# Kernel optimization log

Hardware: AMD Instinct MI355X
Metric: run time of the kernel (lower is better)

The kernel has to match this reference:

```python
import jax, jax.numpy as jnp
import numpy as np

D_MODEL = 96
D_INNER = 192   # ssm_ratio * d_model
R = 6           # dt_rank = ceil(96/16)
DH = 32         # d_inner // dt_rank (per-head dim)
K = 4           # scan directions
N = 16          # d_state
EPS = 1e-5


def setup_inputs() -> dict:
    key = jax.random.key(0)
    ks = jax.random.split(key, 10)
    B, H, W = 8, 64, 64
    f = lambda k, s, sc: jax.random.normal(k, s, jnp.float32) * sc
    return dict(
        x=jax.random.normal(ks[0], (B, H, W, D_MODEL), jnp.float32),
        w_in=f(ks[1], (D_MODEL, D_INNER), 0.02),
        w_conv=f(ks[2], (3, 3, 1, D_INNER), 0.1),      # depthwise HWIO
        b_conv=f(ks[3], (D_INNER,), 0.1),
        x_proj_weight=f(ks[4], (K, R + 2 * N, D_INNER), 0.02),
        A_logs=f(ks[5], (K, R), 0.5),
        Ds=jnp.ones((K, R, DH), jnp.float32),
        dt_bias=0.1 * jax.random.uniform(ks[6], (K, R), jnp.float32),
        ln_g=jnp.ones((D_INNER,), jnp.float32),
        ln_b=jnp.zeros((D_INNER,), jnp.float32),
        w_out=f(ks[7], (D_INNER, D_MODEL), 0.02),
    )


def _cross_scan(x):
    # x: (B,H,W,C) -> (B,L,4,C): [row-major, col-major, rev row, rev col]
    B, H, W, C = x.shape
    x0 = x.reshape(B, H * W, C)
    x1 = jnp.transpose(x, (0, 2, 1, 3)).reshape(B, H * W, C)
    return jnp.stack([x0, x1, x0[:, ::-1], x1[:, ::-1]], axis=2)


def _cross_merge(ys, H, W):
    # ys: (B,L,4,C) -> (B,L,C) summed after undoing each scan order
    B, L, _, C = ys.shape
    y_row = ys[:, :, 0] + ys[:, :, 2][:, ::-1]
    y_col = ys[:, :, 1] + ys[:, :, 3][:, ::-1]
    y_col = jnp.transpose(y_col.reshape(B, W, H, C), (0, 2, 1, 3)).reshape(B, L, C)
    return y_row + y_col


def _selective_scan(us, dts, As, Bs, Cs, Dsr, dtb):
    # us:(B,L,KR,DH) dts:(B,L,KR) As:(KR,) Bs,Cs:(B,L,K,N) Dsr:(KR,DH) dtb:(KR,)
    dt = jax.nn.softplus(dts + dtb)                 # (B,L,KR)
    decay = jnp.exp(dt * As)                        # (B,L,KR)
    xu = dt[..., None] * us                         # (B,L,KR,DH)
    Bh = jnp.repeat(Bs, R, axis=2)                  # (B,L,KR,N) head h -> group h//R
    Ch = jnp.repeat(Cs, R, axis=2)
    B_, L, KR, _ = us.shape
    tfirst = lambda a: jnp.moveaxis(a, 1, 0)

    def step(h, inp):
        dec, xu_t, b_t, c_t = inp                   # (B,KR),(B,KR,DH),(B,KR,N),(B,KR,N)
        h = dec[:, :, None, None] * h + xu_t[..., None] * b_t[:, :, None, :]
        y = jnp.einsum('bkdn,bkn->bkd', h, c_t)
        return h, y

    h0 = jnp.zeros((B_, KR, DH, N), us.dtype)
    _, ys = jax.lax.scan(step, h0, (tfirst(decay), tfirst(xu), tfirst(Bh), tfirst(Ch)))
    ys = jnp.moveaxis(ys, 0, 1)                     # (B,L,KR,DH)
    return ys + us * Dsr                            # skip term D*u


def reference(x, w_in, w_conv, b_conv, x_proj_weight, A_logs, Ds, dt_bias, ln_g, ln_b, w_out):
    B, H, W, _ = x.shape
    L = H * W
    xi = x @ w_in                                   # in_proj (no bias)
    xi = jax.lax.conv_general_dilated(
        xi, w_conv, (1, 1), 'SAME', feature_group_count=D_INNER,
        dimension_numbers=('NHWC', 'HWIO', 'NHWC')) + b_conv
    xi = jax.nn.silu(xi)
    xs = _cross_scan(xi)                            # (B,L,4,D_INNER)
    x_dbl = jnp.einsum('blkd,kcd->blkc', xs, x_proj_weight)
    dts = x_dbl[..., :R].reshape(B, L, K * R)
    Bs = x_dbl[..., R:R + N]                        # (B,L,K,N)
    Cs = x_dbl[..., R + N:]
    us = xs.reshape(B, L, K * R, DH)
    As = -jnp.exp(A_logs.astype(jnp.float32)).reshape(K * R)
    Dsr = Ds.reshape(K * R, DH)
    dtb = dt_bias.reshape(K * R)
    ys = _selective_scan(us, dts, As, Bs, Cs, Dsr, dtb)   # (B,L,KR,DH)
    y = _cross_merge(ys.reshape(B, L, K, R * DH), H, W)   # (B,L,D_INNER)
    mu = y.mean(-1, keepdims=True)
    var = ((y - mu) ** 2).mean(-1, keepdims=True)
    y = (y - mu) / jnp.sqrt(var + EPS) * ln_g + ln_b
    y = y.reshape(B, H, W, D_INNER)
    return y @ w_out                                # out_proj (no bias)
```

## Files before the change

### kernel.cpp

```cpp
#include <hip/hip_runtime.h>
#include <hip/hip_bf16.h>

#define BB 8
#define LL 4096
#define DM 96
#define DI 192
#define RRR 6
#define DHH 32
#define KKK 4
#define NNN 16
#define KRR 24
#define NCH 64
#define TT 64
#define RST 48

__device__ __forceinline__ float softplus_f(float x){
    float ax = fabsf(x);
    return fmaxf(x, 0.f) + __logf(1.f + __expf(-ax));
}
__device__ __forceinline__ float silu_f(float x){ return x / (1.f + __expf(-x)); }

__global__ void k0p(const float* __restrict__ W, const float* __restrict__ g,
                    const float* __restrict__ bta, const float* __restrict__ w_out,
                    float* __restrict__ WpR, float* __restrict__ wg, float* __restrict__ sgbw){
    int i = blockIdx.x * 256 + threadIdx.x;
    if (i < DI * 160){
        int d = i / 160, cc = i % 160; int gq = cc / 40, nc = cc % 40;
        int dir = (gq == 0) ? 0 : (gq == 1) ? 2 : (gq == 2) ? 1 : 3;
        float v = 0.f;
        if (nc < 6) v = W[(dir * 38 + nc) * DI + d];
        else if (nc >= 8) v = W[(dir * 38 + (nc - 2)) * DI + d];
        WpR[i] = v;
    } else if (i < DI * 160 + DI * DM){
        int j = i - DI * 160; int c = j / DM;
        wg[j] = w_out[j] * g[c];
    } else if (i < DI * 160 + DI * DM + DM){
        int m = i - (DI * 160 + DI * DM);
        float s = 0.f, t = 0.f;
        for (int c = 0; c < DI; ++c){
            float w = w_out[c * DM + m];
            s = fmaf(g[c], w, s);
            t = fmaf(bta[c], w, t);
        }
        sgbw[m] = s; sgbw[DM + m] = t;
    }
}

__global__ __launch_bounds__(384) void k1_inproj(const float* __restrict__ x,
                                                 const float* __restrict__ w_in,
                                                 float* __restrict__ xw){
    __shared__ float xT[DM][36];
    int pix0 = blockIdx.x * 32;
    for (int i = threadIdx.x; i < 32 * 24; i += 384){
        int c4 = i % 24, p = i / 24;
        float4 v = *(const float4*)(x + (size_t)(pix0 + p) * DM + c4 * 4);
        xT[c4 * 4 + 0][p] = v.x; xT[c4 * 4 + 1][p] = v.y;
        xT[c4 * 4 + 2][p] = v.z; xT[c4 * 4 + 3][p] = v.w;
    }
    __syncthreads();
    int cg = threadIdx.x % 48, pg = threadIdx.x / 48;
    int p0 = pg * 4;
    float4 acc[4];
    #pragma unroll
    for (int i = 0; i < 4; ++i) acc[i] = make_float4(0.f, 0.f, 0.f, 0.f);
    const float* wcol = w_in + cg * 4;
    for (int d0 = 0; d0 < DM; d0 += 8){
        float4 wv[8], xv[8];
        #pragma unroll
        for (int j = 0; j < 8; ++j){
            wv[j] = *(const float4*)(wcol + (d0 + j) * DI);
            xv[j] = *(const float4*)(&xT[d0 + j][p0]);
        }
        #pragma unroll
        for (int j = 0; j < 8; ++j){
            float xs[4] = {xv[j].x, xv[j].y, xv[j].z, xv[j].w};
            #pragma unroll
            for (int pi = 0; pi < 4; ++pi){
                acc[pi].x = fmaf(xs[pi], wv[j].x, acc[pi].x);
                acc[pi].y = fmaf(xs[pi], wv[j].y, acc[pi].y);
                acc[pi].z = fmaf(xs[pi], wv[j].z, acc[pi].z);
                acc[pi].w = fmaf(xs[pi], wv[j].w, acc[pi].w);
            }
        }
    }
    #pragma unroll
    for (int pi = 0; pi < 4; ++pi)
        *(float4*)(xw + (size_t)(pix0 + p0 + pi) * DI + cg * 4) = acc[pi];
}

__global__ void k2_conv(const float* __restrict__ xw, const float* __restrict__ wc,
                        const float* __restrict__ bc, float* __restrict__ xi,
                        float* __restrict__ xiT){
    int gid = blockIdx.x * 256 + threadIdx.x;
    int c4 = gid % 48; int pix = gid / 48;
    int b = pix >> 12; int l = pix & 4095; int h = l >> 6; int w = l & 63;
    int c = c4 * 4;
    float4 acc = *(const float4*)(bc + c);
    #pragma unroll
    for (int dh = 0; dh < 3; ++dh){
        int hh = h + dh - 1; if ((unsigned)hh >= 64u) continue;
        #pragma unroll
        for (int dw = 0; dw < 3; ++dw){
            int ww2 = w + dw - 1; if ((unsigned)ww2 >= 64u) continue;
            float4 tap = *(const float4*)(xw + (size_t)((b << 12) + (hh << 6) + ww2) * DI + c);
            float4 wv  = *(const float4*)(wc + (dh * 3 + dw) * DI + c);
            acc.x = fmaf(tap.x, wv.x, acc.x);
            acc.y = fmaf(tap.y, wv.y, acc.y);
            acc.z = fmaf(tap.z, wv.z, acc.z);
            acc.w = fmaf(tap.w, wv.w, acc.w);
        }
    }
    acc.x = silu_f(acc.x); acc.y = silu_f(acc.y); acc.z = silu_f(acc.z); acc.w = silu_f(acc.w);
    *(float4*)(xi + (size_t)pix * DI + c) = acc;
    int lT = ((l & 63) << 6) | (l >> 6);
    *(float4*)(xiT + (size_t)((b << 12) + lT) * DI + c) = acc;
}

__global__ __launch_bounds__(320) void k3seq(const float* __restrict__ xi,
                                             const float* __restrict__ xiT,
                                             const float* __restrict__ WpR,
                                             const float* __restrict__ A_logs,
                                             const float* __restrict__ dtb,
                                             float* __restrict__ rec){
    __shared__ float xT[96][68];
    int z = blockIdx.y, b = blockIdx.z;
    int l0 = blockIdx.x * 64;
    const float* src = (z ? xiT : xi) + ((((size_t)b) << 12) + l0) * DI;
    int kg = threadIdx.x % 20, pg = threadIdx.x / 20;
    int p0 = pg * 4;
    float4 acc[4];
    #pragma unroll
    for (int i = 0; i < 4; ++i) acc[i] = make_float4(0.f, 0.f, 0.f, 0.f);
    const float* wcol = WpR + z * 80 + kg * 4;
    #pragma unroll
    for (int half = 0; half < 2; ++half){
        __syncthreads();
        for (int i = threadIdx.x; i < 64 * 24; i += 320){
            int c4 = i % 24, p = i / 24;
            float4 v = *(const float4*)(src + (size_t)p * DI + half * 96 + c4 * 4);
            xT[c4 * 4 + 0][p] = v.x; xT[c4 * 4 + 1][p] = v.y;
            xT[c4 * 4 + 2][p] = v.z; xT[c4 * 4 + 3][p] = v.w;
        }
        __syncthreads();
        const float* wp = wcol + half * 96 * 160;
        for (int d0 = 0; d0 < 96; d0 += 8){
            float4 wv[8], xv[8];
            #pragma unroll
            for (int j = 0; j < 8; ++j){
                wv[j] = *(const float4*)(wp + (d0 + j) * 160);
                xv[j] = *(const float4*)(&xT[d0 + j][p0]);
            }
            #pragma unroll
            for (int j = 0; j < 8; ++j){
                float xs[4] = {xv[j].x, xv[j].y, xv[j].z, xv[j].w};
                #pragma unroll
                for (int pi = 0; pi < 4; ++pi){
                    acc[pi].x = fmaf(xs[pi], wv[j].x, acc[pi].x);
                    acc[pi].y = fmaf(xs[pi], wv[j].y, acc[pi].y);
                    acc[pi].z = fmaf(xs[pi], wv[j].z, acc[pi].z);
                    acc[pi].w = fmaf(xs[pi], wv[j].w, acc[pi].w);
                }
            }
        }
    }
    int sub = kg / 10;
    int dir = (z == 0) ? (sub == 0 ? 0 : 2) : (sub == 0 ? 1 : 3);
    int nc0 = (kg % 10) * 4;
    float* rb = rec + (size_t)(b * KKK + dir) * LL * RST;
    float A0 = 0.f, A1 = 0.f, A2 = 0.f, A3 = 0.f, b0 = 0.f, b1 = 0.f, b2 = 0.f, b3 = 0.f;
    if (nc0 == 0){
        A0 = -__expf(A_logs[dir * RRR + 0]); b0 = dtb[dir * RRR + 0];
        A1 = -__expf(A_logs[dir * RRR + 1]); b1 = dtb[dir * RRR + 1];
        A2 = -__expf(A_logs[dir * RRR + 2]); b2 = dtb[dir * RRR + 2];
        A3 = -__expf(A_logs[dir * RRR + 3]); b3 = dtb[dir * RRR + 3];
    } else if (nc0 == 4){
        A0 = -__expf(A_logs[dir * RRR + 4]); b0 = dtb[dir * RRR + 4];
        A1 = -__expf(A_logs[dir * RRR + 5]); b1 = dtb[dir * RRR + 5];
    }
    #pragma unroll
    for (int pi = 0; pi < 4; ++pi){
        int l = l0 + p0 + pi;
        int t = (sub == 0) ? l : (LL - 1 - l);
        float* rw = rb + (size_t)t * RST;
        float4 v = acc[pi];
        if (nc0 == 0){
            float4 dt4, dc4;
            dt4.x = softplus_f(v.x + b0); dc4.x = __expf(dt4.x * A0);
            dt4.y = softplus_f(v.y + b1); dc4.y = __expf(dt4.y * A1);
            dt4.z = softplus_f(v.z + b2); dc4.z = __expf(dt4.z * A2);
            dt4.w = softplus_f(v.w + b3); dc4.w = __expf(dt4.w * A3);
            *(float4*)(rw + 0) = dt4;
            *(float4*)(rw + 8) = dc4;
        } else if (nc0 == 4){
            float4 dt4, dc4;
            dt4.x = softplus_f(v.x + b0); dc4.x = __expf(dt4.x * A0);
            dt4.y = softplus_f(v.y + b1); dc4.y = __expf(dt4.y * A1);
            dt4.z = 0.f; dt4.w = 0.f; dc4.z = 0.f; dc4.w = 0.f;
            *(float4*)(rw + 4)  = dt4;
            *(float4*)(rw + 12) = dc4;
        } else {
            *(float4*)(rw + nc0 + 8) = v;
        }
    }
}

__global__ __launch_bounds__(192) void k4a(const float* __restrict__ xi, const float* __restrict__ xiT,
                                           const float* __restrict__ rec,
                                           float* __restrict__ Pb, float* __restrict__ Sb){
    int chunk = blockIdx.x, k = blockIdx.y, b = blockIdx.z;
    int r = threadIdx.x >> 5, d = threadIdx.x & 31;
    int kr = k * RRR + r;
    const float* rp = rec + ((size_t)(b * KKK + k) * LL + chunk * TT) * RST;
    const float* xb = ((k & 1) ? xiT : xi) + (((size_t)b) << 12) * DI + r * DHH + d;
    const float* up; ptrdiff_t ust;
    if (k < 2){ up = xb + (size_t)(chunk * TT) * DI;          ust = DI;  }
    else      { up = xb + (size_t)(LL - 1 - chunk * TT) * DI; ust = -(ptrdiff_t)DI; }
    float h[NNN];
    #pragma unroll
    for (int n = 0; n < NNN; ++n) h[n] = 0.f;
    float P = 1.f;
    #pragma unroll 4
    for (int tt = 0; tt < TT; ++tt){
        float dt  = rp[r];
        float dec = rp[8 + r];
        float u = *up;
        float xu = dt * u;
        P *= dec;
        float Bv[NNN];
        *(float4*)(Bv + 0)  = *(const float4*)(rp + 16);
        *(float4*)(Bv + 4)  = *(const float4*)(rp + 20);
        *(float4*)(Bv + 8)  = *(const float4*)(rp + 24);
        *(float4*)(Bv + 12) = *(const float4*)(rp + 28);
        #pragma unroll
        for (int n = 0; n < NNN; ++n) h[n] = fmaf(dec, h[n], xu * Bv[n]);
        rp += RST; up += ust;
    }
    size_t sb = (((size_t)(b * KRR + kr) * NCH + chunk) * DHH + d) * NNN;
    #pragma unroll
    for (int n = 0; n < NNN; ++n) Sb[sb + n] = h[n];
    if (d == 0) Pb[(size_t)(b * KRR + kr) * NCH + chunk] = P;
}

__global__ __launch_bounds__(256) void k4b(const float* __restrict__ Pb, float* __restrict__ Sb){
    int scan = blockIdx.x >> 1;
    int half = blockIdx.x & 1;
    int tid = half * 256 + threadIdx.x;
    size_t base = (size_t)scan * NCH * 512 + tid;
    const float* Pp = Pb + (size_t)scan * NCH;
    float s[NCH];
    #pragma unroll
    for (int c = 0; c < NCH; ++c) s[c] = Sb[base + (size_t)c * 512];
    float hb = 0.f;
    #pragma unroll
    for (int c = 0; c < NCH; ++c){
        float nv = fmaf(Pp[c], hb, s[c]);
        Sb[base + (size_t)c * 512] = hb;
        hb = nv;
    }
}

__global__ __launch_bounds__(192) void k4c(const float* __restrict__ xi, const float* __restrict__ xiT,
                                           const float* __restrict__ rec,
                                           const float* __restrict__ Ds, const float* __restrict__ Sb,
                                           __hip_bfloat16* __restrict__ ybuf){
    int chunk = blockIdx.x, k = blockIdx.y, b = blockIdx.z;
    int r = threadIdx.x >> 5, d = threadIdx.x & 31;
    int kr = k * RRR + r;
    float Dv = Ds[kr * DHH + d];
    float h[NNN];
    size_t sb = (((size_t)(b * KRR + kr) * NCH + chunk) * DHH + d) * NNN;
    #pragma unroll
    for (int n = 0; n < NNN; ++n) h[n] = Sb[sb + n];
    const float* rp = rec + ((size_t)(b * KKK + k) * LL + chunk * TT) * RST;
    const float* xb = ((k & 1) ? xiT : xi) + (((size_t)b) << 12) * DI + r * DHH + d;
    const float* up; ptrdiff_t ust;
    if (k < 2){ up = xb + (size_t)(chunk * TT) * DI;          ust = DI;  }
    else      { up = xb + (size_t)(LL - 1 - chunk * TT) * DI; ust = -(ptrdiff_t)DI; }
    __hip_bfloat16* yp = ybuf + ((size_t)(k * BB + b) * LL + chunk * TT) * DI + r * DHH + d;
    #pragma unroll 2
    for (int tt = 0; tt < TT; ++tt){
        float dt  = rp[r];
        float dec = rp[8 + r];
        float u = *up;
        float xu = dt * u;
        float Bv[NNN], Cv[NNN];
        *(float4*)(Bv + 0)  = *(const float4*)(rp + 16);
        *(float4*)(Bv + 4)  = *(const float4*)(rp + 20);
        *(float4*)(Bv + 8)  = *(const float4*)(rp + 24);
        *(float4*)(Bv + 12) = *(const float4*)(rp + 28);
        *(float4*)(Cv + 0)  = *(const float4*)(rp + 32);
        *(float4*)(Cv + 4)  = *(const float4*)(rp + 36);
        *(float4*)(Cv + 8)  = *(const float4*)(rp + 40);
        *(float4*)(Cv + 12) = *(const float4*)(rp + 44);
        float y = 0.f;
        #pragma unroll
        for (int n = 0; n < NNN; ++n){
            h[n] = fmaf(dec, h[n], xu * Bv[n]);
            y = fmaf(h[n], Cv[n], y);
        }
        y = fmaf(u, Dv, y);
        *yp = __float2bfloat16(y);
        rp += RST; up += ust; yp += DI;
    }
}

__global__ __launch_bounds__(256) void k5_out(const __hip_bfloat16* __restrict__ ybuf,
                       const float* __restrict__ wg, const float* __restrict__ sgbw,
                       float* __restrict__ out){
    __shared__ float yT[DI][36];
    __shared__ float rsL[32], rmL[32];
    int pix0 = blockIdx.x * 32;
    int b = pix0 >> 12;
    int l0 = pix0 & 4095;
    const __hip_bfloat16* y0 = ybuf + (size_t)(0 * BB + b) * LL * DI;
    const __hip_bfloat16* y1 = ybuf + (size_t)(1 * BB + b) * LL * DI;
    const __hip_bfloat16* y2 = ybuf + (size_t)(2 * BB + b) * LL * DI;
    const __hip_bfloat16* y3 = ybuf + (size_t)(3 * BB + b) * LL * DI;
    for (int i = threadIdx.x; i < 32 * DI; i += 256){
        int c = i % DI, p = i / DI;
        int l = l0 + p; int hh = l >> 6, ww = l & 63;
        int lT = (ww << 6) | hh;
        float s = __bfloat162float(y0[(size_t)l * DI + c])
                + __bfloat162float(y2[(size_t)(LL - 1 - l) * DI + c])
                + __bfloat162float(y1[(size_t)lT * DI + c])
                + __bfloat162float(y3[(size_t)(LL - 1 - lT) * DI + c]);
        yT[c][p] = s;
    }
    __syncthreads();
    {
        int p = threadIdx.x >> 3, cg = threadIdx.x & 7;
        float s = 0.f, s2 = 0.f;
        for (int c = cg; c < DI; c += 8){ float v = yT[c][p]; s += v; s2 = fmaf(v, v, s2); }
        s += __shfl_xor(s, 1, 64); s2 += __shfl_xor(s2, 1, 64);
        s += __shfl_xor(s, 2, 64); s2 += __shfl_xor(s2, 2, 64);
        s += __shfl_xor(s, 4, 64); s2 += __shfl_xor(s2, 4, 64);
        if (cg == 0){
            float mu = s * (1.f / DI);
            float var = s2 * (1.f / DI) - mu * mu;
            float rs = rsqrtf(var + 1e-5f);
            rsL[p] = rs; rmL[p] = rs * mu;
        }
    }
    __syncthreads();
    if (threadIdx.x < 192){
        int mg = threadIdx.x % 24, pg = threadIdx.x / 24;
        int p0 = pg * 4;
        float4 acc[4];
        #pragma unroll
        for (int i = 0; i < 4; ++i) acc[i] = make_float4(0.f, 0.f, 0.f, 0.f);
        const float* wcol = wg + mg * 4;
        for (int c0 = 0; c0 < DI; c0 += 8){
            float4 wv[8], yv[8];
            #pragma unroll
            for (int j = 0; j < 8; ++j){
                wv[j] = *(const float4*)(wcol + (c0 + j) * DM);
                yv[j] = *(const float4*)(&yT[c0 + j][p0]);
            }
            #pragma unroll
            for (int j = 0; j < 8; ++j){
                float ys[4] = {yv[j].x, yv[j].y, yv[j].z, yv[j].w};
                #pragma unroll
                for (int pi = 0; pi < 4; ++pi){
                    acc[pi].x = fmaf(ys[pi], wv[j].x, acc[pi].x);
                    acc[pi].y = fmaf(ys[pi], wv[j].y, acc[pi].y);
                    acc[pi].z = fmaf(ys[pi], wv[j].z, acc[pi].z);
                    acc[pi].w = fmaf(ys[pi], wv[j].w, acc[pi].w);
                }
            }
        }
        float4 sg4 = *(const float4*)(sgbw + mg * 4);
        float4 bw4 = *(const float4*)(sgbw + DM + mg * 4);
        #pragma unroll
        for (int pi = 0; pi < 4; ++pi){
            float rs = rsL[p0 + pi], rm = rmL[p0 + pi];
            float4 o;
            o.x = fmaf(acc[pi].x, rs, fmaf(-rm, sg4.x, bw4.x));
            o.y = fmaf(acc[pi].y, rs, fmaf(-rm, sg4.y, bw4.y));
            o.z = fmaf(acc[pi].z, rs, fmaf(-rm, sg4.z, bw4.z));
            o.w = fmaf(acc[pi].w, rs, fmaf(-rm, sg4.w, bw4.w));
            *(float4*)(out + (size_t)(pix0 + p0 + pi) * DM + mg * 4) = o;
        }
    }
}

extern "C" void kernel_launch(void* const* d_in, const int* in_sizes, int n_in,
                              void* d_out, int out_size, void* d_ws, size_t ws_size,
                              hipStream_t stream){
    const float* x      = (const float*)d_in[0];
    const float* w_in   = (const float*)d_in[1];
    const float* w_conv = (const float*)d_in[2];
    const float* b_conv = (const float*)d_in[3];
    const float* xproj  = (const float*)d_in[4];
    const float* A_logs = (const float*)d_in[5];
    const float* Ds     = (const float*)d_in[6];
    const float* dtbias = (const float*)d_in[7];
    const float* ln_g   = (const float*)d_in[8];
    const float* ln_b   = (const float*)d_in[9];
    const float* w_out  = (const float*)d_in[10];
    float* out = (float*)d_out;

    float* ws   = (float*)d_ws;
    float* xi   = ws;
    float* xiT  = xi + 6291456;
    float* Sb   = xiT + 6291456;
    float* Pb   = Sb + 6291456;
    float* WpR  = Pb + 16384;
    float* wg   = WpR + 30720;
    float* sgbw = wg + 18432;
    float* big  = sgbw + 192;
    float* xw   = big;
    float* rec  = big;
    __hip_bfloat16* ybuf = (__hip_bfloat16*)(big + 6291456);

    k0p<<<193, 256, 0, stream>>>(xproj, ln_g, ln_b, w_out, WpR, wg, sgbw);
    k1_inproj<<<1024, 384, 0, stream>>>(x, w_in, xw);
    k2_conv<<<6144, 256, 0, stream>>>(xw, w_conv, b_conv, xi, xiT);
    k3seq<<<dim3(64, 2, BB), 320, 0, stream>>>(xi, xiT, WpR, A_logs, dtbias, rec);
    k4a<<<dim3(NCH, KKK, BB), 192, 0, stream>>>(xi, xiT, rec, Pb, Sb);
    k4b<<<384, 256, 0, stream>>>(Pb, Sb);
    k4c<<<dim3(NCH, KKK, BB), 192, 0, stream>>>(xi, xiT, rec, Ds, Sb, ybuf);
    k5_out<<<1024, 256, 0, stream>>>(ybuf, wg, sgbw, out);
}
```

Baseline: 283.7 us.

## Use split-bf16 MFMA for x_proj GEMM in k3seq

Replaces the scalar FP32 FMA projection in k3seq with bf16 MFMA 16x16x32 instructions. Each operand is split into high and low bf16 parts and combined with three MFMAs, keeping close to FP32 accuracy. The weights are pre-split and stored transposed (n-major, k contiguous) in k0p. Activations are split into shared memory per half. This targets the ALU cost of the projection GEMM, at the price of extra conversion work, triple MFMA count and more scattered scalar epilogue stores.

```diff
diff --git a/kernel.cpp b/kernel.cpp
--- a/kernel.cpp
+++ b/kernel.cpp
@@ -14,28 +14,42 @@
 #define TT 64
 #define RST 48
 
+typedef unsigned short u16;
+typedef __attribute__((ext_vector_type(8))) __bf16 bf16x8;
+typedef __attribute__((ext_vector_type(4))) float f32x4;
+
 __device__ __forceinline__ float softplus_f(float x){
     float ax = fabsf(x);
     return fmaxf(x, 0.f) + __logf(1.f + __expf(-ax));
 }
 __device__ __forceinline__ float silu_f(float x){ return x / (1.f + __expf(-x)); }
 
+__device__ __forceinline__ void split_bf16(float v, u16& h, u16& l){
+    __bf16 hb = (__bf16)v;
+    h = __builtin_bit_cast(u16, hb);
+    float r = v - (float)hb;
+    l = __builtin_bit_cast(u16, (__bf16)r);
+}
+
 __global__ void k0p(const float* __restrict__ W, const float* __restrict__ g,
                     const float* __restrict__ bta, const float* __restrict__ w_out,
-                    float* __restrict__ WpR, float* __restrict__ wg, float* __restrict__ sgbw){
+                    u16* __restrict__ WhB, u16* __restrict__ WlB,
+                    float* __restrict__ wg, float* __restrict__ sgbw){
     int i = blockIdx.x * 256 + threadIdx.x;
-    if (i < DI * 160){
-        int d = i / 160, cc = i % 160; int gq = cc / 40, nc = cc % 40;
-        int dir = (gq == 0) ? 0 : (gq == 1) ? 2 : (gq == 2) ? 1 : 3;
+    if (i < 2 * 80 * 192){
+        int k = i % 192; int n80 = i / 192; int z = n80 / 80; int n = n80 % 80;
+        int sub = n / 40, nc = n % 40;
+        int dir = (z == 0) ? (sub ? 2 : 0) : (sub ? 3 : 1);
         float v = 0.f;
-        if (nc < 6) v = W[(dir * 38 + nc) * DI + d];
-        else if (nc >= 8) v = W[(dir * 38 + (nc - 2)) * DI + d];
-        WpR[i] = v;
-    } else if (i < DI * 160 + DI * DM){
-        int j = i - DI * 160; int c = j / DM;
+        if (nc < 6) v = W[(dir * 38 + nc) * DI + k];
+        else if (nc >= 8) v = W[(dir * 38 + (nc - 2)) * DI + k];
+        u16 h, l; split_bf16(v, h, l);
+        WhB[i] = h; WlB[i] = l;
+    } else if (i < 30720 + DI * DM){
+        int j = i - 30720; int c = j / DM;
         wg[j] = w_out[j] * g[c];
-    } else if (i < DI * 160 + DI * DM + DM){
-        int m = i - (DI * 160 + DI * DM);
+    } else if (i < 30720 + DI * DM + DM){
+        int m = i - (30720 + DI * DM);
         float s = 0.f, t = 0.f;
         for (int c = 0; c < DI; ++c){
             float w = w_out[c * DM + m];
@@ -116,90 +130,80 @@
     *(float4*)(xiT + (size_t)((b << 12) + lT) * DI + c) = acc;
 }
 
-__global__ __launch_bounds__(320) void k3seq(const float* __restrict__ xi,
+__global__ __launch_bounds__(256) void k3seq(const float* __restrict__ xi,
                                              const float* __restrict__ xiT,
-                                             const float* __restrict__ WpR,
+                                             const u16* __restrict__ WhB,
+                                             const u16* __restrict__ WlB,
                                              const float* __restrict__ A_logs,
                                              const float* __restrict__ dtb,
                                              float* __restrict__ rec){
-    __shared__ float xT[96][68];
+    __shared__ u16 Xh[64][104];
+    __shared__ u16 Xl[64][104];
     int z = blockIdx.y, b = blockIdx.z;
     int l0 = blockIdx.x * 64;
     const float* src = (z ? xiT : xi) + ((((size_t)b) << 12) + l0) * DI;
-    int kg = threadIdx.x % 20, pg = threadIdx.x / 20;
-    int p0 = pg * 4;
-    float4 acc[4];
-    #pragma unroll
-    for (int i = 0; i < 4; ++i) acc[i] = make_float4(0.f, 0.f, 0.f, 0.f);
-    const float* wcol = WpR + z * 80 + kg * 4;
+    int wv = threadIdx.x >> 6, lane = threadIdx.x & 63;
+    int quad = lane >> 4, mi = lane & 15;
+    int m0 = wv * 16;
+    f32x4 acc[5];
+    #pragma unroll
+    for (int nt = 0; nt < 5; ++nt) acc[nt] = (f32x4){0.f, 0.f, 0.f, 0.f};
+    const u16* wh = WhB + (size_t)z * 80 * 192;
+    const u16* wl = WlB + (size_t)z * 80 * 192;
     #pragma unroll
     for (int half = 0; half < 2; ++half){
         __syncthreads();
-        for (int i = threadIdx.x; i < 64 * 24; i += 320){
+        for (int i = threadIdx.x; i < 1536; i += 256){
             int c4 = i % 24, p = i / 24;
             float4 v = *(const float4*)(src + (size_t)p * DI + half * 96 + c4 * 4);
-            xT[c4 * 4 + 0][p] = v.x; xT[c4 * 4 + 1][p] = v.y;
-            xT[c4 * 4 + 2][p] = v.z; xT[c4 * 4 + 3][p] = v.w;
+            u16 h0, h1, h2, h3, q0, q1, q2, q3;
+            split_bf16(v.x, h0, q0); split_bf16(v.y, h1, q1);
+            split_bf16(v.z, h2, q2); split_bf16(v.w, h3, q3);
+            *(ushort4*)&Xh[p][c4 * 4] = make_ushort4(h0, h1, h2, h3);
+            *(ushort4*)&Xl[p][c4 * 4] = make_ushort4(q0, q1, q2, q3);
         }
         __syncthreads();
-        const float* wp = wcol + half * 96 * 160;
-        for (int d0 = 0; d0 < 96; d0 += 8){
-            float4 wv[8], xv[8];
+        #pragma unroll
+        for (int kt = 0; kt < 3; ++kt){
+            int ko = kt * 32 + quad * 8;
+            bf16x8 ah = *(const bf16x8*)&Xh[m0 + mi][ko];
+            bf16x8 al = *(const bf16x8*)&Xl[m0 + mi][ko];
+            int kg = half * 96 + ko;
             #pragma unroll
-            for (int j = 0; j < 8; ++j){
-                wv[j] = *(const float4*)(wp + (d0 + j) * 160);
-                xv[j] = *(const float4*)(&xT[d0 + j][p0]);
+            for (int nt = 0; nt < 5; ++nt){
+                const size_t woff = (size_t)(nt * 16 + mi) * 192 + kg;
+                bf16x8 bh = *(const bf16x8*)(wh + woff);
+                bf16x8 bl = *(const bf16x8*)(wl + woff);
+                acc[nt] = __builtin_amdgcn_mfma_f32_16x16x32_bf16(ah, bh, acc[nt], 0, 0, 0);
+                acc[nt] = __builtin_amdgcn_mfma_f32_16x16x32_bf16(al, bh, acc[nt], 0, 0, 0);
+                acc[nt] = __builtin_amdgcn_mfma_f32_16x16x32_bf16(ah, bl, acc[nt], 0, 0, 0);
             }
-            #pragma unroll
-            for (int j = 0; j < 8; ++j){
-                float xs[4] = {xv[j].x, xv[j].y, xv[j].z, xv[j].w};
-                #pragma unroll
-                for (int pi = 0; pi < 4; ++pi){
-                    acc[pi].x = fmaf(xs[pi], wv[j].x, acc[pi].x);
-                    acc[pi].y = fmaf(xs[pi], wv[j].y, acc[pi].y);
-                    acc[pi].z = fmaf(xs[pi], wv[j].z, acc[pi].z);
-                    acc[pi].w = fmaf(xs[pi], wv[j].w, acc[pi].w);
-                }
+        }
+    }
+    #pragma unroll
+    for (int nt = 0; nt < 5; ++nt){
+        int nc = nt * 16 + mi;
+        int sub = nc / 40;
+        int dir = (z == 0) ? (sub ? 2 : 0) : (sub ? 3 : 1);
+        int c40 = nc % 40;
+        float* rb = rec + (size_t)(b * KKK + dir) * LL * RST;
+        bool isdt = (c40 < 6);
+        bool ispad = (c40 == 6) | (c40 == 7);
+        float Ac = 0.f, bc = 0.f;
+        if (isdt){ Ac = -__expf(A_logs[dir * RRR + c40]); bc = dtb[dir * RRR + c40]; }
+        #pragma unroll
+        for (int i = 0; i < 4; ++i){
+            int l = l0 + m0 + quad * 4 + i;
+            int t = (sub == 0) ? l : (LL - 1 - l);
+            float v = acc[nt][i];
+            float* rw = rb + (size_t)t * RST;
+            if (isdt){
+                float dt = softplus_f(v + bc);
+                rw[c40] = dt;
+                rw[c40 + 8] = __expf(dt * Ac);
+            } else if (!ispad){
+                rw[c40 + 8] = v;
             }
-        }
-    }
-    int sub = kg / 10;
-    int dir = (z == 0) ? (sub == 0 ? 0 : 2) : (sub == 0 ? 1 : 3);
-    int nc0 = (kg % 10) * 4;
-    float* rb = rec + (size_t)(b * KKK + dir) * LL * RST;
-    float A0 = 0.f, A1 = 0.f, A2 = 0.f, A3 = 0.f, b0 = 0.f, b1 = 0.f, b2 = 0.f, b3 = 0.f;
-    if (nc0 == 0){
-        A0 = -__expf(A_logs[dir * RRR + 0]); b0 = dtb[dir * RRR + 0];
-        A1 = -__expf(A_logs[dir * RRR + 1]); b1 = dtb[dir * RRR + 1];
-        A2 = -__expf(A_logs[dir * RRR + 2]); b2 = dtb[dir * RRR + 2];
-        A3 = -__expf(A_logs[dir * RRR + 3]); b3 = dtb[dir * RRR + 3];
-    } else if (nc0 == 4){
-        A0 = -__expf(A_logs[dir * RRR + 4]); b0 = dtb[dir * RRR + 4];
-        A1 = -__expf(A_logs[dir * RRR + 5]); b1 = dtb[dir * RRR + 5];
-    }
-    #pragma unroll
-    for (int pi = 0; pi < 4; ++pi){
-        int l = l0 + p0 + pi;
-        int t = (sub == 0) ? l : (LL - 1 - l);
-        float* rw = rb + (size_t)t * RST;
-        float4 v = acc[pi];
-        if (nc0 == 0){
-            float4 dt4, dc4;
-            dt4.x = softplus_f(v.x + b0); dc4.x = __expf(dt4.x * A0);
-            dt4.y = softplus_f(v.y + b1); dc4.y = __expf(dt4.y * A1);
-            dt4.z = softplus_f(v.z + b2); dc4.z = __expf(dt4.z * A2);
-            dt4.w = softplus_f(v.w + b3); dc4.w = __expf(dt4.w * A3);
-            *(float4*)(rw + 0) = dt4;
-            *(float4*)(rw + 8) = dc4;
-        } else if (nc0 == 4){
-            float4 dt4, dc4;
-            dt4.x = softplus_f(v.x + b0); dc4.x = __expf(dt4.x * A0);
-            dt4.y = softplus_f(v.y + b1); dc4.y = __expf(dt4.y * A1);
-            dt4.z = 0.f; dt4.w = 0.f; dc4.z = 0.f; dc4.w = 0.f;
-            *(float4*)(rw + 4)  = dt4;
-            *(float4*)(rw + 12) = dc4;
-        } else {
-            *(float4*)(rw + nc0 + 8) = v;
         }
     }
 }
@@ -404,18 +408,20 @@
     float* xiT  = xi + 6291456;
     float* Sb   = xiT + 6291456;
     float* Pb   = Sb + 6291456;
-    float* WpR  = Pb + 16384;
-    float* wg   = WpR + 30720;
+    float* wbase= Pb + 16384;
+    u16*   WhB  = (u16*)wbase;
+    u16*   WlB  = (u16*)(wbase + 15360);
+    float* wg   = wbase + 30720;
     float* sgbw = wg + 18432;
     float* big  = sgbw + 192;
     float* xw   = big;
     float* rec  = big;
     __hip_bfloat16* ybuf = (__hip_bfloat16*)(big + 6291456);
 
-    k0p<<<193, 256, 0, stream>>>(xproj, ln_g, ln_b, w_out, WpR, wg, sgbw);
+    k0p<<<193, 256, 0, stream>>>(xproj, ln_g, ln_b, w_out, WhB, WlB, wg, sgbw);
     k1_inproj<<<1024, 384, 0, stream>>>(x, w_in, xw);
     k2_conv<<<6144, 256, 0, stream>>>(xw, w_conv, b_conv, xi, xiT);
-    k3seq<<<dim3(64, 2, BB), 320, 0, stream>>>(xi, xiT, WpR, A_logs, dtbias, rec);
+    k3seq<<<dim3(64, 2, BB), 256, 0, stream>>>(xi, xiT, WhB, WlB, A_logs, dtbias, rec);
     k4a<<<dim3(NCH, KKK, BB), 192, 0, stream>>>(xi, xiT, rec, Pb, Sb);
     k4b<<<384, 256, 0, stream>>>(Pb, Sb);
     k4c<<<dim3(NCH, KKK, BB), 192, 0, stream>>>(xi, xiT, rec, Ds, Sb, ybuf);
```

New measurement: 276.7 us. -2.4%, faster.
